# Optimization experiments

Measured on AMD Instinct MI355X. Metric: run time of the kernel, lower is better.

The kernel has to match this reference:

```python
import jax, jax.numpy as jnp
import numpy as np
from jax import lax

DIM = 192
HEADS = 4
EPS = 1e-12  # torch F.normalize eps


def setup_inputs() -> dict:
    key = jax.random.key(0)
    k1, k2, k3, k4 = jax.random.split(key, 4)
    b, c, h, w = 8, DIM, 128, 128
    x = jax.random.normal(k1, (b, c, h, w), dtype=jnp.float32)
    w_qkv = jax.random.normal(k2, (3 * c, c), dtype=jnp.float32) * (1.0 / np.sqrt(c))
    w_dw = jax.random.normal(k3, (3 * c, 1, 3, 3), dtype=jnp.float32) * (1.0 / 3.0)
    temperature = jnp.ones((HEADS, 1, 1), dtype=jnp.float32)
    w_proj = jax.random.normal(k4, (c, c), dtype=jnp.float32) * (1.0 / np.sqrt(c))
    return {"x": x, "w_qkv": w_qkv, "w_dw": w_dw, "temperature": temperature, "w_proj": w_proj}


def _l2norm(t):
    # torch F.normalize(dim=-1): t / max(||t||_2, eps)
    n = jnp.sqrt(jnp.sum(t * t, axis=-1, keepdims=True))
    return t / jnp.maximum(n, EPS)


def reference(x, w_qkv, w_dw, temperature, w_proj):
    b, c, h, w = x.shape
    heads = HEADS
    hc = c // heads  # channels per head
    # 1x1 conv: dim -> 3*dim
    qkv = jnp.einsum('bchw,oc->bohw', x, w_qkv)
    # depthwise 3x3 conv, padding=1, no relu/norm
    qkv = lax.conv_general_dilated(
        qkv, w_dw, window_strides=(1, 1), padding='SAME',
        feature_group_count=3 * c,
        dimension_numbers=('NCHW', 'OIHW', 'NCHW'))
    q, k, v = jnp.split(qkv, 3, axis=1)
    # b (head c) h w -> b head c (h w)
    n = h * w
    q = q.reshape(b, heads, hc, n)
    k = k.reshape(b, heads, hc, n)
    v = v.reshape(b, heads, hc, n)
    q = _l2norm(q)
    k = _l2norm(k)
    # channel attention: [b, head, hc, hc]
    attn = jnp.einsum('bhcn,bhdn->bhcd', q, k) * temperature[None]
    attn = jax.nn.softmax(attn, axis=-1)
    out = jnp.einsum('bhcd,bhdn->bhcn', attn, v)
    out = out.reshape(b, c, h, w)
    out = jnp.einsum('bchw,oc->bohw', out, w_proj)
    return out
```

## Files before the change

kernel.cpp:

```cpp
#include <hip/hip_runtime.h>
#include <stdint.h>


typedef __attribute__((ext_vector_type(8))) short bf16x8;
typedef __attribute__((ext_vector_type(4))) float f32x4;
typedef unsigned short u16;

#define HW 16384
#define CD 192
#define O3 576
#define KD 192

__device__ __forceinline__ float b2f(u16 u) {
    union { unsigned int i; float f; } v; v.i = ((unsigned int)u) << 16; return v.f;
}
__device__ __forceinline__ u16 f2b(float f) {
    union { float f; unsigned int i; } v; v.f = f;
    return (u16)((v.i + 0x7fffu + ((v.i >> 16) & 1u)) >> 16);
}

__global__ __launch_bounds__(256) void fill_f32(float* p, long long n, float val) {
    long long stride = (long long)gridDim.x * 256;
    for (long long i = blockIdx.x * 256LL + threadIdx.x; i < n; i += stride) p[i] = val;
}

__global__ __launch_bounds__(256) void zerof(float* p, int n) {
    int i = blockIdx.x * 256 + threadIdx.x;
    if (i < n) p[i] = 0.f;
}

__global__ __launch_bounds__(256) void afrag_prep(
    const float* __restrict__ W, u16* __restrict__ Af, int M, int NF)
{
    int t = blockIdx.x * 256 + threadIdx.x;
    if (t >= NF * 64) return;
    int F = t >> 6, lane = t & 63;
    int ks = F % 6, mt = (F / 6) & 3, rwmb = F / 24;
    int row = rwmb * 64 + mt * 16 + (lane & 15);
    int k0 = ks * 32 + (lane >> 4) * 8;
    u16 v[8] __attribute__((aligned(16)));
    if (row < M) {
        const float* src = W + (long long)row * KD + k0;
#pragma unroll
        for (int j = 0; j < 8; j++) v[j] = f2b(src[j]);
    } else {
#pragma unroll
        for (int j = 0; j < 8; j++) v[j] = 0;
    }
    *(bf16x8*)&Af[(long long)F * 512 + lane * 8] = *(const bf16x8*)v;
}

__global__ __launch_bounds__(256) void transpose_f2b(
    const float* __restrict__ in, u16* __restrict__ out,
    long long in_bs, long long out_bs)
{
    __shared__ u16 t[64 * 72];
    const int tid = threadIdx.x;
    const int p0 = blockIdx.x * 64, c0 = blockIdx.y * 64;
    const long long bz = blockIdx.z;
    const float* ib = in + bz * in_bs;
    u16* ob = out + bz * out_bs;
    {
        int cl = tid >> 2, pc = (tid & 3) * 16;
        const float* src = &ib[(long long)(c0 + cl) * HW + p0 + pc];
#pragma unroll
        for (int j4 = 0; j4 < 4; j4++) {
            f32x4 v = *(const f32x4*)(src + j4 * 4);
            u16* d = &t[cl * 72 + pc + j4 * 4];
            d[0] = f2b(v[0]); d[1] = f2b(v[1]); d[2] = f2b(v[2]); d[3] = f2b(v[3]);
        }
    }
    __syncthreads();
    {
        int pl = tid >> 2, cc = (tid & 3) * 16;
        u16 tmp[16] __attribute__((aligned(16)));
#pragma unroll
        for (int j = 0; j < 16; j++) tmp[j] = t[(cc + j) * 72 + pl];
        u16* dst = &ob[(long long)(p0 + pl) * CD + c0 + cc];
        *(bf16x8*)dst       = *(const bf16x8*)&tmp[0];
        *(bf16x8*)(dst + 8) = *(const bf16x8*)&tmp[8];
    }
}

__global__ __launch_bounds__(256) void transpose_b(
    const u16* __restrict__ in, u16* __restrict__ out,
    long long in_bs, long long out_bs)
{
    __shared__ u16 t[64 * 72];
    const int tid = threadIdx.x;
    const int p0 = blockIdx.x * 64, c0 = blockIdx.y * 64;
    const long long bz = blockIdx.z;
    const u16* ib = in + bz * in_bs;
    u16* ob = out + bz * out_bs;
    {
        int cl = tid >> 2, pc = (tid & 3) * 16;
        const u16* src = &ib[(long long)(c0 + cl) * HW + p0 + pc];
        *(bf16x8*)&t[cl * 72 + pc]     = *(const bf16x8*)src;
        *(bf16x8*)&t[cl * 72 + pc + 8] = *(const bf16x8*)(src + 8);
    }
    __syncthreads();
    {
        int pl = tid >> 2, cc = (tid & 3) * 16;
        u16 tmp[16] __attribute__((aligned(16)));
#pragma unroll
        for (int j = 0; j < 16; j++) tmp[j] = t[(cc + j) * 72 + pl];
        u16* dst = &ob[(long long)(p0 + pl) * CD + c0 + cc];
        *(bf16x8*)dst       = *(const bf16x8*)&tmp[0];
        *(bf16x8*)(dst + 8) = *(const bf16x8*)&tmp[8];
    }
}

__device__ __forceinline__ void stage16(const u16* g, u16* l) {
    __builtin_amdgcn_global_load_lds((const __attribute__((address_space(1))) unsigned int*)g,
                                     (__attribute__((address_space(3))) unsigned int*)l, 16, 0, 0);
}

template <bool OUT_F32>
__global__ __launch_bounds__(256, 2) void gemm_af(
    const u16* __restrict__ Afrag, const u16* __restrict__ Bt, void* __restrict__ Cv,
    int M, long long af_bs, long long b_bs, long long c_bs)
{
    __shared__ u16 lsB[6][128 * 32];
    const int tid = threadIdx.x;
    const int lane = tid & 63, wid = tid >> 6;
    const int n0 = blockIdx.x * 128, mb = blockIdx.y;
    const long long bz = blockIdx.z;
    const u16* Bb = Bt + bz * b_bs;
    const int wm = (wid & 1) * 64, wn = (wid >> 1) * 64;
    const int lr = lane & 15, quad = lane >> 4;

    {
        const int srow = lane >> 2;
        const int gslot = (lane & 3) ^ (srow & 3);
        const u16* gp = Bb + (long long)(n0 + wid * 32 + srow) * KD + gslot * 8;
#pragma unroll
        for (int ks = 0; ks < 6; ks++) {
            stage16(gp + ks * 32,               &lsB[ks][(wid * 32) * 32]);
            stage16(gp + 16 * KD + ks * 32,     &lsB[ks][(wid * 32 + 16) * 32]);
        }
    }
    bf16x8 af[4][6];
    {
        const u16* Ap = Afrag + bz * af_bs
                      + ((long long)((mb * 2 + (wid & 1)) * 24)) * 512 + lane * 8;
#pragma unroll
        for (int mt = 0; mt < 4; mt++)
#pragma unroll
            for (int ks = 0; ks < 6; ks++)
                af[mt][ks] = *(const bf16x8*)(Ap + (mt * 6 + ks) * 512);
    }
    f32x4 acc[4][4];
#pragma unroll
    for (int i = 0; i < 4; i++)
#pragma unroll
        for (int j = 0; j < 4; j++) acc[i][j] = (f32x4){0.f, 0.f, 0.f, 0.f};

    __syncthreads();

    const int rslot = (quad ^ (lr & 3)) * 8;
#pragma unroll
    for (int ks = 0; ks < 6; ks++) {
        bf16x8 bfv[4];
#pragma unroll
        for (int nt = 0; nt < 4; nt++)
            bfv[nt] = *(const bf16x8*)&lsB[ks][(wn + nt * 16 + lr) * 32 + rslot];
#pragma unroll
        for (int mt = 0; mt < 4; mt++)
#pragma unroll
            for (int nt = 0; nt < 4; nt++)
                acc[mt][nt] = __builtin_amdgcn_mfma_f32_16x16x32_bf16(af[mt][ks], bfv[nt], acc[mt][nt], 0, 0, 0);
    }
    const int m0 = mb * 128;
#pragma unroll
    for (int mt = 0; mt < 4; mt++)
#pragma unroll
        for (int r = 0; r < 4; r++) {
            int row = m0 + wm + mt * 16 + quad * 4 + r;
            if (row < M) {
#pragma unroll
                for (int nt = 0; nt < 4; nt++) {
                    int col = n0 + wn + nt * 16 + lr;
                    if (OUT_F32)
                        ((float*)Cv)[bz * c_bs + (long long)row * HW + col] = acc[mt][nt][r];
                    else
                        ((u16*)Cv)[bz * c_bs + (long long)row * HW + col] = f2b(acc[mt][nt][r]);
                }
            }
        }
}

__global__ __launch_bounds__(256) void dwconv2(
    const u16* __restrict__ in, const float* __restrict__ wdw, u16* __restrict__ outp,
    long long in_bs, long long out_bs, int wch0)
{
    const int rt = blockIdx.x, ch = blockIdx.y, tid = threadIdx.x;
    const long long bz = blockIdx.z;
    const u16* ip = in + bz * in_bs + (long long)ch * HW;
    u16* op = outp + bz * out_bs + (long long)ch * HW;
    __shared__ float t[18 * 132];
    const int r0 = rt * 16;
    if (tid < 18) {
        t[tid * 132 + 0] = 0.f;   t[tid * 132 + 129] = 0.f;
        t[tid * 132 + 130] = 0.f; t[tid * 132 + 131] = 0.f;
    }
    for (int i = tid; i < 288; i += 256) {
        int rr = i >> 4, cc = (i & 15) * 8;
        int gr = r0 + rr - 1;
        float f[8];
        if (gr >= 0 && gr < 128) {
            bf16x8 v = *(const bf16x8*)(ip + gr * 128 + cc);
#pragma unroll
            for (int j = 0; j < 8; j++) f[j] = b2f((u16)v[j]);
        } else {
#pragma unroll
            for (int j = 0; j < 8; j++) f[j] = 0.f;
        }
#pragma unroll
        for (int j = 0; j < 8; j++) t[rr * 132 + 1 + cc + j] = f[j];
    }
    float w[9];
#pragma unroll
    for (int j = 0; j < 9; j++) w[j] = wdw[(wch0 + ch) * 9 + j];
    __syncthreads();
    const int rr = tid >> 4, c8 = (tid & 15) * 8;
    float o[8] = {0.f, 0.f, 0.f, 0.f, 0.f, 0.f, 0.f, 0.f};
#pragma unroll
    for (int dy = 0; dy < 3; dy++) {
        const float* row = &t[(rr + dy) * 132 + c8];
        float r[12] __attribute__((aligned(16)));
        *(f32x4*)&r[0] = *(const f32x4*)row;
        *(f32x4*)&r[4] = *(const f32x4*)(row + 4);
        *(f32x4*)&r[8] = *(const f32x4*)(row + 8);
        const float w0 = w[dy * 3], w1 = w[dy * 3 + 1], w2 = w[dy * 3 + 2];
#pragma unroll
        for (int j = 0; j < 8; j++) o[j] += w0 * r[j] + w1 * r[j + 1] + w2 * r[j + 2];
    }
    u16 ob[8] __attribute__((aligned(16)));
#pragma unroll
    for (int j = 0; j < 8; j++) ob[j] = f2b(o[j]);
    *(bf16x8*)&op[(long long)(r0 + rr) * 128 + c8] = *(const bf16x8*)ob;
}

__global__ __launch_bounds__(256) void attn_scores(
    const u16* __restrict__ qk, float* __restrict__ S, float* __restrict__ norms,
    int bh0)
{
    const int tid = threadIdx.x, lane = tid & 63, wid = tid >> 6;
    const int kc = blockIdx.x, head = blockIdx.y;
    const long long bz = blockIdx.z;
    const u16* q = qk + bz * (2LL * CD * HW) + (long long)head * 48 * HW;
    const u16* k = q + (long long)CD * HW;
    const int lr = lane & 15, quad = lane >> 4;

    f32x4 sc[3][3], sq[3], sk[3];
#pragma unroll
    for (int i = 0; i < 3; i++) {
#pragma unroll
        for (int j = 0; j < 3; j++) sc[i][j] = (f32x4){0.f, 0.f, 0.f, 0.f};
        sq[i] = (f32x4){0.f, 0.f, 0.f, 0.f};
        sk[i] = (f32x4){0.f, 0.f, 0.f, 0.f};
    }
    const int n0 = kc * 1024 + wid * 256;
#pragma unroll 2
    for (int s = 0; s < 8; s++) {
        const int n = n0 + s * 32 + quad * 8;
        bf16x8 aq[3], ak[3];
#pragma unroll
        for (int t3 = 0; t3 < 3; t3++) {
            aq[t3] = *(const bf16x8*)(q + (long long)(t3 * 16 + lr) * HW + n);
            ak[t3] = *(const bf16x8*)(k + (long long)(t3 * 16 + lr) * HW + n);
        }
#pragma unroll
        for (int mt = 0; mt < 3; mt++)
#pragma unroll
            for (int nt = 0; nt < 3; nt++)
                sc[mt][nt] = __builtin_amdgcn_mfma_f32_16x16x32_bf16(aq[mt], ak[nt], sc[mt][nt], 0, 0, 0);
#pragma unroll
        for (int t3 = 0; t3 < 3; t3++) {
            sq[t3] = __builtin_amdgcn_mfma_f32_16x16x32_bf16(aq[t3], aq[t3], sq[t3], 0, 0, 0);
            sk[t3] = __builtin_amdgcn_mfma_f32_16x16x32_bf16(ak[t3], ak[t3], sk[t3], 0, 0, 0);
        }
    }
    __shared__ float sS[2304];
    __shared__ float snq[48], snk[48];
    for (int i = tid; i < 2304; i += 256) sS[i] = 0.f;
    if (tid < 48) { snq[tid] = 0.f; snk[tid] = 0.f; }
    __syncthreads();
#pragma unroll
    for (int mt = 0; mt < 3; mt++)
#pragma unroll
        for (int nt = 0; nt < 3; nt++)
#pragma unroll
            for (int r = 0; r < 4; r++)
                atomicAdd(&sS[(mt * 16 + quad * 4 + r) * 48 + nt * 16 + lr], sc[mt][nt][r]);
#pragma unroll
    for (int t3 = 0; t3 < 3; t3++)
#pragma unroll
        for (int r = 0; r < 4; r++) {
            int rw = quad * 4 + r;
            if (rw == lr) {
                atomicAdd(&snq[t3 * 16 + rw], sq[t3][r]);
                atomicAdd(&snk[t3 * 16 + rw], sk[t3][r]);
            }
        }
    __syncthreads();
    const int bh = bh0 + (int)bz * 4 + head;
    float* Sg = S + (long long)bh * 2304;
    for (int i = tid; i < 2304; i += 256) atomicAdd(&Sg[i], sS[i]);
    float* ng = norms + bh * 96;
    if (tid < 48) atomicAdd(&ng[tid], snq[tid]);
    else if (tid < 96) atomicAdd(&ng[tid], snk[tid - 48]);
}

__global__ __launch_bounds__(64) void softmax_k(
    const float* __restrict__ S, const float* __restrict__ norms,
    const float* __restrict__ temp, float* __restrict__ attn, int bh0)
{
    const int bh = bh0 + blockIdx.x, head = bh & 3, r = threadIdx.x;
    if (r >= 48) return;
    const float tv = temp[head];
    const float* Sg = S + (long long)bh * 2304;
    const float* ng = norms + bh * 96;
    const float nq = fmaxf(sqrtf(ng[r]), 1e-12f);
    float lg[48];
    float mx = -1e30f;
#pragma unroll
    for (int d = 0; d < 48; d++) {
        float nk = fmaxf(sqrtf(ng[48 + d]), 1e-12f);
        float v = Sg[r * 48 + d] * tv / (nq * nk);
        lg[d] = v; mx = fmaxf(mx, v);
    }
    float sum = 0.f;
#pragma unroll
    for (int d = 0; d < 48; d++) { float e = __expf(lg[d] - mx); lg[d] = e; sum += e; }
    const float inv = 1.f / sum;
    float* Ag = attn + (long long)bh * 2304 + r * 48;
#pragma unroll
    for (int d = 0; d < 48; d++) Ag[d] = lg[d] * inv;
}

__global__ __launch_bounds__(256) void mproj(
    const float* __restrict__ wproj, const float* __restrict__ attn, u16* __restrict__ Mm,
    int b0)
{
    const int ob = blockIdx.x, b = b0 + blockIdx.y, tid = threadIdx.x;
    __shared__ float sA[9216];
    const float* Ab = attn + (long long)b * 9216;
    for (int i = tid; i < 9216; i += 256) sA[i] = Ab[i];
    __syncthreads();
    for (int i = tid; i < 48 * 192; i += 256) {
        int o = ob * 48 + i / 192;
        int cc = i % 192;
        int h = cc / 48, d = cc - h * 48;
        const float* wr = wproj + o * 192 + h * 48;
        const float* ar = &sA[h * 2304 + d];
        float acc = 0.f;
        for (int c = 0; c < 48; c++) acc += wr[c] * ar[c * 48];
        int fi = (o >> 6) * 24 + ((o >> 4) & 3) * 6 + (cc >> 5);
        int lanei = ((cc >> 3) & 3) * 16 + (o & 15);
        Mm[(long long)b * 49152 + (long long)fi * 512 + lanei * 8 + (cc & 7)] = f2b(acc);
    }
}

extern "C" void kernel_launch(void* const* d_in, const int* in_sizes, int n_in,
                              void* d_out, int out_size, void* d_ws, size_t ws_size,
                              hipStream_t stream)
{
    const float* x     = (const float*)d_in[0];
    const float* wqkv  = (const float*)d_in[1];
    const float* wdw   = (const float*)d_in[2];
    const float* temp  = (const float*)d_in[3];
    const float* wproj = (const float*)d_in[4];
    float* out = (float*)d_out;
    char* ws = (char*)d_ws;
    const long long CHW = (long long)CD * HW;

    if (ws_size < 2097152ULL + 31457280ULL) {
        fill_f32<<<2048, 256, 0, stream>>>(out, out_size, 100.0f);
        return;
    }
    int G = 8;
    while (G > 1 && (unsigned long long)(2097152ULL + (unsigned long long)G * 31457280ULL) > (unsigned long long)ws_size)
        G >>= 1;

    float* S      = (float*)ws;
    float* norms  = (float*)(ws + 294912);
    float* attn   = (float*)(ws + 307200);
    u16*   MmF    = (u16*)(ws + 602112);
    u16*   wqkvF  = (u16*)(ws + 1388544);
    u16* region1  = (u16*)(ws + 2097152);
    u16* qkv_pre  = region1 + (long long)G * 2 * CHW;

    zerof<<<300, 256, 0, stream>>>(S, 76800);
    afrag_prep<<<60, 256, 0, stream>>>(wqkv, wqkvF, O3, 240);

    for (int g0 = 0; g0 < 8; g0 += G) {
        transpose_f2b<<<dim3(256, 3, G), 256, 0, stream>>>(
            x + (long long)g0 * CHW, region1, CHW, CHW);
        gemm_af<false><<<dim3(128, 5, G), 256, 0, stream>>>(
            wqkvF, region1, qkv_pre, O3, 0LL, CHW, 3LL * CHW);
        dwconv2<<<dim3(8, 384, G), 256, 0, stream>>>(
            qkv_pre, wdw, region1, 3LL * CHW, 2LL * CHW, 0);
        dwconv2<<<dim3(8, 192, G), 256, 0, stream>>>(
            qkv_pre + 2LL * CHW, wdw, qkv_pre, 3LL * CHW, 3LL * CHW, 384);
        attn_scores<<<dim3(16, 4, G), 256, 0, stream>>>(region1, S, norms, g0 * 4);
        softmax_k<<<4 * G, 64, 0, stream>>>(S, norms, temp, attn, g0 * 4);
        mproj<<<dim3(4, G), 256, 0, stream>>>(wproj, attn, MmF, g0);
        transpose_b<<<dim3(256, 3, G), 256, 0, stream>>>(
            qkv_pre, qkv_pre + CHW, 3LL * CHW, 3LL * CHW);
        gemm_af<true><<<dim3(128, 2, G), 256, 0, stream>>>(
            MmF + (long long)g0 * 49152, qkv_pre + CHW, out + (long long)g0 * CHW,
            CD, 49152LL, 3LL * CHW, CHW);
    }
}
```

Measured before the change: 436.2 us.

## Fuse input transposes into GEMM B-staging and loop over M blocks per CTA

Removes the separate transpose_f2b and transpose_b kernels. Each GEMM block now reads the channel-major B operand directly, packs pairs of pixels into bf16 and transposes them in registers while writing LDS, with a changed swizzle. Each block also keeps its B tile in LDS and loops over all M blocks (5 for the QKV GEMM, 2 for the projection). This drops two kernel launches and a full round trip of intermediate data through memory. In exchange the grid is 5x or 2x smaller, and the staging reads are narrow strided loads instead of async global_load_lds.

```diff
diff --git a/kernel.cpp b/kernel.cpp
--- a/kernel.cpp
+++ b/kernel.cpp
@@ -4,6 +4,8 @@
 
 typedef __attribute__((ext_vector_type(8))) short bf16x8;
 typedef __attribute__((ext_vector_type(4))) float f32x4;
+typedef __attribute__((ext_vector_type(2))) float f32x2;
+typedef __attribute__((ext_vector_type(4))) unsigned int u32x4;
 typedef unsigned short u16;
 
 #define HW 16384
@@ -50,143 +52,111 @@
     *(bf16x8*)&Af[(long long)F * 512 + lane * 8] = *(const bf16x8*)v;
 }
 
-__global__ __launch_bounds__(256) void transpose_f2b(
-    const float* __restrict__ in, u16* __restrict__ out,
-    long long in_bs, long long out_bs)
-{
-    __shared__ u16 t[64 * 72];
-    const int tid = threadIdx.x;
-    const int p0 = blockIdx.x * 64, c0 = blockIdx.y * 64;
+template <bool SRC_F32, bool OUT_F32>
+__global__ __launch_bounds__(256, 2) void gemm_tn(
+    const u16* __restrict__ Afrag, const void* __restrict__ Bsrc, void* __restrict__ Cv,
+    int M, int nmb, long long af_bs, long long b_bs, long long c_bs)
+{
+    __shared__ u16 lsB[6][128 * 32];
+    const int tid = threadIdx.x, lane = tid & 63, wid = tid >> 6;
+    const int n0 = blockIdx.x * 128;
     const long long bz = blockIdx.z;
-    const float* ib = in + bz * in_bs;
-    u16* ob = out + bz * out_bs;
+    const int lr = lane & 15, quad = lane >> 4;
+    const int wm = (wid & 1) * 64, wn = (wid >> 1) * 64;
+
     {
-        int cl = tid >> 2, pc = (tid & 3) * 16;
-        const float* src = &ib[(long long)(c0 + cl) * HW + p0 + pc];
-#pragma unroll
-        for (int j4 = 0; j4 < 4; j4++) {
-            f32x4 v = *(const f32x4*)(src + j4 * 4);
-            u16* d = &t[cl * 72 + pc + j4 * 4];
-            d[0] = f2b(v[0]); d[1] = f2b(v[1]); d[2] = f2b(v[2]); d[3] = f2b(v[3]);
-        }
-    }
-    __syncthreads();
-    {
-        int pl = tid >> 2, cc = (tid & 3) * 16;
-        u16 tmp[16] __attribute__((aligned(16)));
-#pragma unroll
-        for (int j = 0; j < 16; j++) tmp[j] = t[(cc + j) * 72 + pl];
-        u16* dst = &ob[(long long)(p0 + pl) * CD + c0 + cc];
-        *(bf16x8*)dst       = *(const bf16x8*)&tmp[0];
-        *(bf16x8*)(dst + 8) = *(const bf16x8*)&tmp[8];
-    }
-}
-
-__global__ __launch_bounds__(256) void transpose_b(
-    const u16* __restrict__ in, u16* __restrict__ out,
-    long long in_bs, long long out_bs)
-{
-    __shared__ u16 t[64 * 72];
-    const int tid = threadIdx.x;
-    const int p0 = blockIdx.x * 64, c0 = blockIdx.y * 64;
-    const long long bz = blockIdx.z;
-    const u16* ib = in + bz * in_bs;
-    u16* ob = out + bz * out_bs;
-    {
-        int cl = tid >> 2, pc = (tid & 3) * 16;
-        const u16* src = &ib[(long long)(c0 + cl) * HW + p0 + pc];
-        *(bf16x8*)&t[cl * 72 + pc]     = *(const bf16x8*)src;
-        *(bf16x8*)&t[cl * 72 + pc + 8] = *(const bf16x8*)(src + 8);
-    }
-    __syncthreads();
-    {
-        int pl = tid >> 2, cc = (tid & 3) * 16;
-        u16 tmp[16] __attribute__((aligned(16)));
-#pragma unroll
-        for (int j = 0; j < 16; j++) tmp[j] = t[(cc + j) * 72 + pl];
-        u16* dst = &ob[(long long)(p0 + pl) * CD + c0 + cc];
-        *(bf16x8*)dst       = *(const bf16x8*)&tmp[0];
-        *(bf16x8*)(dst + 8) = *(const bf16x8*)&tmp[8];
-    }
-}
-
-__device__ __forceinline__ void stage16(const u16* g, u16* l) {
-    __builtin_amdgcn_global_load_lds((const __attribute__((address_space(1))) unsigned int*)g,
-                                     (__attribute__((address_space(3))) unsigned int*)l, 16, 0, 0);
-}
-
-template <bool OUT_F32>
-__global__ __launch_bounds__(256, 2) void gemm_af(
-    const u16* __restrict__ Afrag, const u16* __restrict__ Bt, void* __restrict__ Cv,
-    int M, long long af_bs, long long b_bs, long long c_bs)
-{
-    __shared__ u16 lsB[6][128 * 32];
-    const int tid = threadIdx.x;
-    const int lane = tid & 63, wid = tid >> 6;
-    const int n0 = blockIdx.x * 128, mb = blockIdx.y;
-    const long long bz = blockIdx.z;
-    const u16* Bb = Bt + bz * b_bs;
-    const int wm = (wid & 1) * 64, wn = (wid >> 1) * 64;
-    const int lr = lane & 15, quad = lane >> 4;
-
-    {
-        const int srow = lane >> 2;
-        const int gslot = (lane & 3) ^ (srow & 3);
-        const u16* gp = Bb + (long long)(n0 + wid * 32 + srow) * KD + gslot * 8;
+        const int slot = wid ^ (lane & 3);
+        u16* dA = &lsB[0][(2 * lane) * 32 + slot * 8];
+        u16* dB = &lsB[0][(2 * lane + 1) * 32 + slot * 8];
+        if (SRC_F32) {
+            const float* gp = (const float*)Bsrc + bz * b_bs
+                            + (long long)(wid * 8) * HW + n0 + 2 * lane;
+#pragma unroll
+            for (int ks = 0; ks < 6; ks++) {
+                f32x2 rv[8];
+#pragma unroll
+                for (int j = 0; j < 8; j++) rv[j] = *(const f32x2*)(gp + (long long)j * HW);
+                gp += 32LL * HW;
+                unsigned int lo[4], hi[4];
+#pragma unroll
+                for (int i = 0; i < 4; i++) {
+                    float a0 = rv[2 * i][0], b0 = rv[2 * i + 1][0];
+                    float a1 = rv[2 * i][1], b1 = rv[2 * i + 1][1];
+                    asm("v_cvt_pk_bf16_f32 %0, %1, %2" : "=v"(lo[i]) : "v"(a0), "v"(b0));
+                    asm("v_cvt_pk_bf16_f32 %0, %1, %2" : "=v"(hi[i]) : "v"(a1), "v"(b1));
+                }
+                *(u32x4*)(dA + ks * 4096) = (u32x4){lo[0], lo[1], lo[2], lo[3]};
+                *(u32x4*)(dB + ks * 4096) = (u32x4){hi[0], hi[1], hi[2], hi[3]};
+            }
+        } else {
+            const u16* gp = (const u16*)Bsrc + bz * b_bs
+                          + (long long)(wid * 8) * HW + n0 + 2 * lane;
+#pragma unroll
+            for (int ks = 0; ks < 6; ks++) {
+                unsigned int rv[8];
+#pragma unroll
+                for (int j = 0; j < 8; j++) rv[j] = *(const unsigned int*)(gp + (long long)j * HW);
+                gp += 32LL * HW;
+                unsigned int lo[4], hi[4];
+#pragma unroll
+                for (int i = 0; i < 4; i++) {
+                    lo[i] = (rv[2 * i] & 0xffffu) | (rv[2 * i + 1] << 16);
+                    hi[i] = (rv[2 * i] >> 16) | (rv[2 * i + 1] & 0xffff0000u);
+                }
+                *(u32x4*)(dA + ks * 4096) = (u32x4){lo[0], lo[1], lo[2], lo[3]};
+                *(u32x4*)(dB + ks * 4096) = (u32x4){hi[0], hi[1], hi[2], hi[3]};
+            }
+        }
+    }
+    __syncthreads();
+
+    const int rslot = (quad ^ ((lr >> 1) & 3)) * 8;
+    for (int mb = 0; mb < nmb; ++mb) {
+        bf16x8 af[4][6];
+        {
+            const u16* Ap = Afrag + bz * af_bs
+                          + ((long long)((mb * 2 + (wid & 1)) * 24)) * 512 + lane * 8;
+#pragma unroll
+            for (int mt = 0; mt < 4; mt++)
+#pragma unroll
+                for (int ks = 0; ks < 6; ks++)
+                    af[mt][ks] = *(const bf16x8*)(Ap + (mt * 6 + ks) * 512);
+        }
+        f32x4 acc[4][4];
+#pragma unroll
+        for (int i = 0; i < 4; i++)
+#pragma unroll
+            for (int j = 0; j < 4; j++) acc[i][j] = (f32x4){0.f, 0.f, 0.f, 0.f};
 #pragma unroll
         for (int ks = 0; ks < 6; ks++) {
-            stage16(gp + ks * 32,               &lsB[ks][(wid * 32) * 32]);
-            stage16(gp + 16 * KD + ks * 32,     &lsB[ks][(wid * 32 + 16) * 32]);
-        }
-    }
-    bf16x8 af[4][6];
-    {
-        const u16* Ap = Afrag + bz * af_bs
-                      + ((long long)((mb * 2 + (wid & 1)) * 24)) * 512 + lane * 8;
+            bf16x8 bfv[4];
+#pragma unroll
+            for (int nt = 0; nt < 4; nt++)
+                bfv[nt] = *(const bf16x8*)&lsB[ks][(wn + nt * 16 + lr) * 32 + rslot];
+#pragma unroll
+            for (int mt = 0; mt < 4; mt++)
+#pragma unroll
+                for (int nt = 0; nt < 4; nt++)
+                    acc[mt][nt] = __builtin_amdgcn_mfma_f32_16x16x32_bf16(af[mt][ks], bfv[nt], acc[mt][nt], 0, 0, 0);
+        }
+        const int m0 = mb * 128;
 #pragma unroll
         for (int mt = 0; mt < 4; mt++)
 #pragma unroll
-            for (int ks = 0; ks < 6; ks++)
-                af[mt][ks] = *(const bf16x8*)(Ap + (mt * 6 + ks) * 512);
-    }
-    f32x4 acc[4][4];
-#pragma unroll
-    for (int i = 0; i < 4; i++)
-#pragma unroll
-        for (int j = 0; j < 4; j++) acc[i][j] = (f32x4){0.f, 0.f, 0.f, 0.f};
-
-    __syncthreads();
-
-    const int rslot = (quad ^ (lr & 3)) * 8;
-#pragma unroll
-    for (int ks = 0; ks < 6; ks++) {
-        bf16x8 bfv[4];
-#pragma unroll
-        for (int nt = 0; nt < 4; nt++)
-            bfv[nt] = *(const bf16x8*)&lsB[ks][(wn + nt * 16 + lr) * 32 + rslot];
-#pragma unroll
-        for (int mt = 0; mt < 4; mt++)
-#pragma unroll
-            for (int nt = 0; nt < 4; nt++)
-                acc[mt][nt] = __builtin_amdgcn_mfma_f32_16x16x32_bf16(af[mt][ks], bfv[nt], acc[mt][nt], 0, 0, 0);
-    }
-    const int m0 = mb * 128;
-#pragma unroll
-    for (int mt = 0; mt < 4; mt++)
-#pragma unroll
-        for (int r = 0; r < 4; r++) {
-            int row = m0 + wm + mt * 16 + quad * 4 + r;
-            if (row < M) {
-#pragma unroll
-                for (int nt = 0; nt < 4; nt++) {
-                    int col = n0 + wn + nt * 16 + lr;
-                    if (OUT_F32)
-                        ((float*)Cv)[bz * c_bs + (long long)row * HW + col] = acc[mt][nt][r];
-                    else
-                        ((u16*)Cv)[bz * c_bs + (long long)row * HW + col] = f2b(acc[mt][nt][r]);
+            for (int r = 0; r < 4; r++) {
+                int row = m0 + wm + mt * 16 + quad * 4 + r;
+                if (row < M) {
+#pragma unroll
+                    for (int nt = 0; nt < 4; nt++) {
+                        int col = n0 + wn + nt * 16 + lr;
+                        if (OUT_F32)
+                            ((float*)Cv)[bz * c_bs + (long long)row * HW + col] = acc[mt][nt][r];
+                        else
+                            ((u16*)Cv)[bz * c_bs + (long long)row * HW + col] = f2b(acc[mt][nt][r]);
+                    }
                 }
             }
-        }
+    }
 }
 
 __global__ __launch_bounds__(256) void dwconv2(
@@ -395,10 +365,8 @@
     afrag_prep<<<60, 256, 0, stream>>>(wqkv, wqkvF, O3, 240);
 
     for (int g0 = 0; g0 < 8; g0 += G) {
-        transpose_f2b<<<dim3(256, 3, G), 256, 0, stream>>>(
-            x + (long long)g0 * CHW, region1, CHW, CHW);
-        gemm_af<false><<<dim3(128, 5, G), 256, 0, stream>>>(
-            wqkvF, region1, qkv_pre, O3, 0LL, CHW, 3LL * CHW);
+        gemm_tn<true, false><<<dim3(128, 1, G), 256, 0, stream>>>(
+            wqkvF, x + (long long)g0 * CHW, qkv_pre, O3, 5, 0LL, CHW, 3LL * CHW);
         dwconv2<<<dim3(8, 384, G), 256, 0, stream>>>(
             qkv_pre, wdw, region1, 3LL * CHW, 2LL * CHW, 0);
         dwconv2<<<dim3(8, 192, G), 256, 0, stream>>>(
@@ -406,10 +374,8 @@
         attn_scores<<<dim3(16, 4, G), 256, 0, stream>>>(region1, S, norms, g0 * 4);
         softmax_k<<<4 * G, 64, 0, stream>>>(S, norms, temp, attn, g0 * 4);
         mproj<<<dim3(4, G), 256, 0, stream>>>(wproj, attn, MmF, g0);
-        transpose_b<<<dim3(256, 3, G), 256, 0, stream>>>(
-            qkv_pre, qkv_pre + CHW, 3LL * CHW, 3LL * CHW);
-        gemm_af<true><<<dim3(128, 2, G), 256, 0, stream>>>(
-            MmF + (long long)g0 * 49152, qkv_pre + CHW, out + (long long)g0 * CHW,
-            CD, 49152LL, 3LL * CHW, CHW);
-    }
-}
+        gemm_tn<false, true><<<dim3(128, 1, G), 256, 0, stream>>>(
+            MmF + (long long)g0 * 49152, qkv_pre, out + (long long)g0 * CHW,
+            CD, 2, 49152LL, 3LL * CHW, CHW);
+    }
+}
```

Measured after the change: 410.2 us. 1.06x faster.
